# Kernel tuning notes

Hardware: AMD Instinct MI355X
Metric: run time of the kernel (lower is better)

Reference implementation:

```python
import jax, jax.numpy as jnp
import numpy as np

N = 100000
E = 800000
D = 128


def setup_inputs() -> dict:
    key = jax.random.key(0)
    k1, k2, k3, k4 = jax.random.split(key, 4)
    x = jax.random.normal(k1, (N, D), dtype=jnp.float32)
    edge_index = jax.random.randint(k2, (2, E), 0, N, dtype=jnp.int64)
    s = 1.0 / np.sqrt(D)
    W1 = jax.random.uniform(k3, (D, D), jnp.float32, -s, s)
    b1 = jnp.zeros((D,), jnp.float32)
    W2 = jax.random.uniform(k4, (D, D), jnp.float32, -s, s)
    b2 = jnp.zeros((D,), jnp.float32)
    return {"x": x, "edge_index": edge_index, "W1": W1, "b1": b1, "W2": W2, "b2": b2}


def _degree(idx, n, dtype):
    return jax.ops.segment_sum(jnp.ones(idx.shape, dtype), idx, num_segments=n)


def _graph_conv(x, row, col, W, b, residual, act):
    n = x.shape[0]
    deg_out = jnp.clip(_degree(row, n, x.dtype), 1.0)          # [N]
    x_src = x * jax.lax.rsqrt(deg_out)[:, None]                # [N, D]
    # scatter-add messages from source (row) into target (col)
    agg = jax.ops.segment_sum(x_src[row], col, num_segments=n)  # [N, D]
    out = agg @ W.T + b
    deg_in = jnp.clip(_degree(col, n, x.dtype), 1.0)
    out = out * jax.lax.rsqrt(deg_in)[:, None]
    if residual:
        out = out + x  # res_fc is Identity (in_dim == out_dim)
    if act:
        out = jax.nn.relu(out)
    return out


def reference(x, edge_index, W1, b1, W2, b2):
    row, col = edge_index[0], edge_index[1]
    # layer 1: relu + residual; layer 2 (last, encoding=False): no act, no residual
    h = _graph_conv(x, row, col, W1, b1, residual=True, act=True)
    h = _graph_conv(h, row, col, W2, b2, residual=False, act=False)
    return h
```

## Files before the change

### kernel.cpp

```cpp
#include <hip/hip_runtime.h>


#define NN 100000
#define EE 800000
#define DD 128
#define NB1 98
#define NTILE (NN / 16)

typedef __attribute__((ext_vector_type(8))) short short8;
typedef __attribute__((ext_vector_type(4))) float floatx4;

__device__ inline float bf2f(unsigned int u16) {
    union { unsigned int i; float f; } c;
    c.i = u16 << 16;
    return c.f;
}
__device__ inline ushort f2bf(float f) {
    union { float f; unsigned int i; } c;
    c.f = f;
    unsigned int u = c.i;
    return (ushort)((u + 0x7fffu + ((u >> 16) & 1u)) >> 16);
}

__global__ __launch_bounds__(256) void count_kernel(const int* __restrict__ row,
                                                    const int* __restrict__ col,
                                                    int* __restrict__ cnt_out,
                                                    int* __restrict__ cnt_in,
                                                    int* __restrict__ off) {
    int e = blockIdx.x * 256 + threadIdx.x;
    if (e < EE) {
        off[e] = atomicAdd(&cnt_in[col[e]], 1);
        atomicAdd(&cnt_out[row[e]], 1);
    }
}

__global__ __launch_bounds__(256) void dinv_kernel(const int* __restrict__ cnt_out,
                                                   const int* __restrict__ cnt_in,
                                                   float* __restrict__ dinv_out,
                                                   float* __restrict__ dinv_in) {
    int n = blockIdx.x * 256 + threadIdx.x;
    if (n < NN) {
        dinv_out[n] = rsqrtf((float)max(cnt_out[n], 1));
        dinv_in[n]  = rsqrtf((float)max(cnt_in[n], 1));
    }
}

__global__ __launch_bounds__(256) void scan1_kernel(const int* __restrict__ cnt,
                                                    int* __restrict__ excl,
                                                    int* __restrict__ bsums) {
    __shared__ int tmp[256];
    const int t = threadIdx.x;
    const int base = blockIdx.x * 1024 + t * 4;
    int a[4];
#pragma unroll
    for (int q = 0; q < 4; ++q) a[q] = (base + q < NN) ? cnt[base + q] : 0;
    int s = a[0] + a[1] + a[2] + a[3];
    tmp[t] = s;
    __syncthreads();
    for (int off = 1; off < 256; off <<= 1) {
        int v = 0;
        if (t >= off) v = tmp[t - off];
        __syncthreads();
        tmp[t] += v;
        __syncthreads();
    }
    int excl_s = tmp[t] - s;
    if (t == 255) bsums[blockIdx.x] = tmp[t];
    int run = excl_s;
#pragma unroll
    for (int q = 0; q < 4; ++q) {
        if (base + q < NN) excl[base + q] = run;
        run += a[q];
    }
}

__global__ __launch_bounds__(256) void scan2_kernel(int* __restrict__ bsums, int nb) {
    __shared__ int tmp[256];
    const int t = threadIdx.x;
    int s = (t < nb) ? bsums[t] : 0;
    tmp[t] = s;
    __syncthreads();
    for (int off = 1; off < 256; off <<= 1) {
        int v = 0;
        if (t >= off) v = tmp[t - off];
        __syncthreads();
        tmp[t] += v;
        __syncthreads();
    }
    if (t < nb) bsums[t] = tmp[t] - s;
}

__global__ __launch_bounds__(256) void scan3_kernel(const int* __restrict__ excl,
                                                    const int* __restrict__ bsums,
                                                    int* __restrict__ row_start) {
    int i = blockIdx.x * 256 + threadIdx.x;
    if (i < NN) row_start[i] = excl[i] + bsums[i >> 10];
}

__global__ __launch_bounds__(256) void fill_kernel(const int* __restrict__ row,
                                                   const int* __restrict__ col,
                                                   const int* __restrict__ row_start,
                                                   const int* __restrict__ off,
                                                   int* __restrict__ srcs) {
    int e = blockIdx.x * 256 + threadIdx.x;
    if (e < EE) srcs[row_start[col[e]] + off[e]] = row[e];
}

__global__ __launch_bounds__(256) void prescale_kernel(const float* __restrict__ x,
                                                       const float* __restrict__ dinv_out,
                                                       ushort* __restrict__ xb) {
    int idx = blockIdx.x * 256 + threadIdx.x;
    if (idx >= NN * 32) return;
    int n = idx >> 5;
    float s = dinv_out[n];
    float4 v = ((const float4*)x)[idx];
    ushort4 o;
    o.x = f2bf(v.x * s);
    o.y = f2bf(v.y * s);
    o.z = f2bf(v.z * s);
    o.w = f2bf(v.w * s);
    ((ushort4*)xb)[idx] = o;
}

__global__ __launch_bounds__(256) void gather_kernel(const ushort* __restrict__ src,
                                                     const int* __restrict__ row_start,
                                                     const int* __restrict__ srcs,
                                                     ushort* __restrict__ agg) {
    const int node = blockIdx.x * 16 + (threadIdx.x >> 4);
    const int lane = threadIdx.x & 15;
    if (node >= NN) return;
    int p = row_start[node];
    const int end = (node + 1 < NN) ? row_start[node + 1] : EE;
    float a0 = 0.f, a1 = 0.f, a2 = 0.f, a3 = 0.f;
    float a4 = 0.f, a5 = 0.f, a6 = 0.f, a7 = 0.f;

#define ACCUM(V)                                     \
    do {                                             \
        a0 += bf2f((V).x & 0xffffu);                 \
        a1 += bf2f((V).x >> 16);                     \
        a2 += bf2f((V).y & 0xffffu);                 \
        a3 += bf2f((V).y >> 16);                     \
        a4 += bf2f((V).z & 0xffffu);                 \
        a5 += bf2f((V).z >> 16);                     \
        a6 += bf2f((V).w & 0xffffu);                 \
        a7 += bf2f((V).w >> 16);                     \
    } while (0)

    for (; p + 3 < end; p += 4) {
        int s0 = srcs[p];
        int s1 = srcs[p + 1];
        int s2 = srcs[p + 2];
        int s3 = srcs[p + 3];
        uint4 v0 = ((const uint4*)(src + (size_t)s0 * DD))[lane];
        uint4 v1 = ((const uint4*)(src + (size_t)s1 * DD))[lane];
        uint4 v2 = ((const uint4*)(src + (size_t)s2 * DD))[lane];
        uint4 v3 = ((const uint4*)(src + (size_t)s3 * DD))[lane];
        ACCUM(v0); ACCUM(v1); ACCUM(v2); ACCUM(v3);
    }
    for (; p < end; ++p) {
        int s0 = srcs[p];
        uint4 v0 = ((const uint4*)(src + (size_t)s0 * DD))[lane];
        ACCUM(v0);
    }
#undef ACCUM

    uint4 o;
    o.x = (unsigned int)f2bf(a0) | ((unsigned int)f2bf(a1) << 16);
    o.y = (unsigned int)f2bf(a2) | ((unsigned int)f2bf(a3) << 16);
    o.z = (unsigned int)f2bf(a4) | ((unsigned int)f2bf(a5) << 16);
    o.w = (unsigned int)f2bf(a6) | ((unsigned int)f2bf(a7) << 16);
    ((uint4*)(agg + (size_t)node * DD))[lane] = o;
}

template <bool L1>
__global__ __launch_bounds__(256) void gemm_ep(const ushort* __restrict__ agg,
                                               const float* __restrict__ W,
                                               const float* __restrict__ bias,
                                               const float* __restrict__ dinv_in,
                                               const float* __restrict__ dinv_out,
                                               const float* __restrict__ x,
                                               ushort* __restrict__ hs,
                                               float* __restrict__ out) {
    __shared__ ushort Ws[128 * 136];
    {
        int j = threadIdx.x >> 1;
        int k0 = (threadIdx.x & 1) * 64;
        const float4* wp = (const float4*)(W + (size_t)j * DD + k0);
        ushort* dst = Ws + j * 136 + k0;
#pragma unroll
        for (int q = 0; q < 16; ++q) {
            float4 v = wp[q];
            ushort4 o;
            o.x = f2bf(v.x); o.y = f2bf(v.y); o.z = f2bf(v.z); o.w = f2bf(v.w);
            *(ushort4*)(dst + q * 4) = o;
        }
    }
    __syncthreads();

    const int wave = threadIdx.x >> 6;
    const int lane = threadIdx.x & 63;
    const int tile = blockIdx.x * 4 + wave;
    if (tile >= NTILE) return;
    const int mi = lane & 15;
    const int quad = lane >> 4;
    const int m0 = tile * 16;

    floatx4 acc[8];
#pragma unroll
    for (int t = 0; t < 8; ++t) acc[t] = (floatx4){0.f, 0.f, 0.f, 0.f};

    const ushort* ap = agg + (size_t)(m0 + mi) * DD + quad * 8;
#pragma unroll
    for (int s = 0; s < 4; ++s) {
        short8 a = *(const short8*)(ap + s * 32);
#pragma unroll
        for (int t = 0; t < 8; ++t) {
            short8 b = *(const short8*)(Ws + (t * 16 + mi) * 136 + s * 32 + quad * 8);
            acc[t] = __builtin_amdgcn_mfma_f32_16x16x32_bf16(a, b, acc[t], 0, 0, 0);
        }
    }

    float dv[4], dov[4];
#pragma unroll
    for (int i = 0; i < 4; ++i) {
        int r = m0 + quad * 4 + i;
        dv[i] = dinv_in[r];
        if (L1) dov[i] = dinv_out[r];
    }
#pragma unroll
    for (int t = 0; t < 8; ++t) {
        int c = t * 16 + mi;
        float bv = bias[c];
#pragma unroll
        for (int i = 0; i < 4; ++i) {
            int r = m0 + quad * 4 + i;
            float o = (acc[t][i] + bv) * dv[i];
            if (L1) {
                o += x[(size_t)r * DD + c];
                o = fmaxf(o, 0.f);
                hs[(size_t)r * DD + c] = f2bf(o * dov[i]);
            } else {
                out[(size_t)r * DD + c] = o;
            }
        }
    }
}

extern "C" void kernel_launch(void* const* d_in, const int* in_sizes, int n_in,
                              void* d_out, int out_size, void* d_ws, size_t ws_size,
                              hipStream_t stream) {
    const float* x  = (const float*)d_in[0];
    const int*   ei = (const int*)d_in[1];
    const float* W1 = (const float*)d_in[2];
    const float* b1 = (const float*)d_in[3];
    const float* W2 = (const float*)d_in[4];
    const float* b2 = (const float*)d_in[5];
    float* out = (float*)d_out;

    const int* row = ei;
    const int* col = ei + EE;

    ushort* agg     = (ushort*)d_ws;
    ushort* xb      = agg + (size_t)NN * DD;
    float* dinv_out = (float*)(xb + (size_t)NN * DD);
    float* dinv_in  = dinv_out + NN;
    int*   cnt      = (int*)(dinv_in + NN);
    int*   excl     = cnt + 2 * NN;
    int*   row_st   = excl + NN;
    int*   srcs     = row_st + NN;
    int*   bsums    = srcs + EE;
    int*   off      = (int*)agg;

    hipMemsetAsync(cnt, 0, 2 * NN * sizeof(int), stream);
    count_kernel<<<(EE + 255) / 256, 256, 0, stream>>>(row, col, cnt, cnt + NN, off);
    dinv_kernel<<<(NN + 255) / 256, 256, 0, stream>>>(cnt, cnt + NN, dinv_out, dinv_in);
    scan1_kernel<<<NB1, 256, 0, stream>>>(cnt + NN, excl, bsums);
    scan2_kernel<<<1, 256, 0, stream>>>(bsums, NB1);
    scan3_kernel<<<(NN + 255) / 256, 256, 0, stream>>>(excl, bsums, row_st);
    fill_kernel<<<(EE + 255) / 256, 256, 0, stream>>>(row, col, row_st, off, srcs);

    prescale_kernel<<<(NN * 32 + 255) / 256, 256, 0, stream>>>(x, dinv_out, xb);
    gather_kernel<<<(NN + 15) / 16, 256, 0, stream>>>(xb, row_st, srcs, agg);
    gemm_ep<true><<<(NTILE + 3) / 4, 256, 0, stream>>>(agg, W1, b1, dinv_in, dinv_out, x,
                                                       xb, nullptr);

    gather_kernel<<<(NN + 15) / 16, 256, 0, stream>>>(xb, row_st, srcs, agg);
    gemm_ep<false><<<(NTILE + 3) / 4, 256, 0, stream>>>(agg, W2, b2, dinv_in, nullptr, nullptr,
                                                        nullptr, out);
}
```

Baseline: 315.1 us.

## Fuse neighbor gather into GEMM epilogue kernel via shared-memory aggregation tile

Merges the gather kernel and the MFMA GEMM kernel into one per-layer kernel. Each block aggregates 64 destination rows into an LDS tile, then runs the bf16 MFMA GEMM from LDS. This removes the global round trip of the aggregation buffer and two launches, and layer 1 now writes into a separate hs buffer. The trade-off is higher LDS use per block, which lowers occupancy, and the whole block waits on its slowest gather row before the GEMM starts.

```diff
diff --git a/kernel.cpp b/kernel.cpp
--- a/kernel.cpp
+++ b/kernel.cpp
@@ -5,7 +5,6 @@
 #define EE 800000
 #define DD 128
 #define NB1 98
-#define NTILE (NN / 16)
 
 typedef __attribute__((ext_vector_type(8))) short short8;
 typedef __attribute__((ext_vector_type(4))) float floatx4;
@@ -122,66 +121,20 @@
     ((ushort4*)xb)[idx] = o;
 }
 
-__global__ __launch_bounds__(256) void gather_kernel(const ushort* __restrict__ src,
-                                                     const int* __restrict__ row_start,
-                                                     const int* __restrict__ srcs,
-                                                     ushort* __restrict__ agg) {
-    const int node = blockIdx.x * 16 + (threadIdx.x >> 4);
-    const int lane = threadIdx.x & 15;
-    if (node >= NN) return;
-    int p = row_start[node];
-    const int end = (node + 1 < NN) ? row_start[node + 1] : EE;
-    float a0 = 0.f, a1 = 0.f, a2 = 0.f, a3 = 0.f;
-    float a4 = 0.f, a5 = 0.f, a6 = 0.f, a7 = 0.f;
-
-#define ACCUM(V)                                     \
-    do {                                             \
-        a0 += bf2f((V).x & 0xffffu);                 \
-        a1 += bf2f((V).x >> 16);                     \
-        a2 += bf2f((V).y & 0xffffu);                 \
-        a3 += bf2f((V).y >> 16);                     \
-        a4 += bf2f((V).z & 0xffffu);                 \
-        a5 += bf2f((V).z >> 16);                     \
-        a6 += bf2f((V).w & 0xffffu);                 \
-        a7 += bf2f((V).w >> 16);                     \
-    } while (0)
-
-    for (; p + 3 < end; p += 4) {
-        int s0 = srcs[p];
-        int s1 = srcs[p + 1];
-        int s2 = srcs[p + 2];
-        int s3 = srcs[p + 3];
-        uint4 v0 = ((const uint4*)(src + (size_t)s0 * DD))[lane];
-        uint4 v1 = ((const uint4*)(src + (size_t)s1 * DD))[lane];
-        uint4 v2 = ((const uint4*)(src + (size_t)s2 * DD))[lane];
-        uint4 v3 = ((const uint4*)(src + (size_t)s3 * DD))[lane];
-        ACCUM(v0); ACCUM(v1); ACCUM(v2); ACCUM(v3);
-    }
-    for (; p < end; ++p) {
-        int s0 = srcs[p];
-        uint4 v0 = ((const uint4*)(src + (size_t)s0 * DD))[lane];
-        ACCUM(v0);
-    }
-#undef ACCUM
-
-    uint4 o;
-    o.x = (unsigned int)f2bf(a0) | ((unsigned int)f2bf(a1) << 16);
-    o.y = (unsigned int)f2bf(a2) | ((unsigned int)f2bf(a3) << 16);
-    o.z = (unsigned int)f2bf(a4) | ((unsigned int)f2bf(a5) << 16);
-    o.w = (unsigned int)f2bf(a6) | ((unsigned int)f2bf(a7) << 16);
-    ((uint4*)(agg + (size_t)node * DD))[lane] = o;
-}
-
 template <bool L1>
-__global__ __launch_bounds__(256) void gemm_ep(const ushort* __restrict__ agg,
-                                               const float* __restrict__ W,
-                                               const float* __restrict__ bias,
-                                               const float* __restrict__ dinv_in,
-                                               const float* __restrict__ dinv_out,
-                                               const float* __restrict__ x,
-                                               ushort* __restrict__ hs,
-                                               float* __restrict__ out) {
+__global__ __launch_bounds__(256) void fused_layer(const ushort* __restrict__ src,
+                                                   const int* __restrict__ row_start,
+                                                   const int* __restrict__ srcs,
+                                                   const float* __restrict__ W,
+                                                   const float* __restrict__ bias,
+                                                   const float* __restrict__ dinv_in,
+                                                   const float* __restrict__ dinv_out,
+                                                   const float* __restrict__ x,
+                                                   ushort* __restrict__ hs,
+                                                   float* __restrict__ out) {
     __shared__ ushort Ws[128 * 136];
+    __shared__ ushort At[64 * 136];
+
     {
         int j = threadIdx.x >> 1;
         int k0 = (threadIdx.x & 1) * 64;
@@ -195,21 +148,68 @@
             *(ushort4*)(dst + q * 4) = o;
         }
     }
+
+    {
+        const int grp  = threadIdx.x >> 4;
+        const int lane = threadIdx.x & 15;
+        const int m0 = blockIdx.x * 64;
+        for (int q = 0; q < 4; ++q) {
+            const int node = m0 + q * 16 + grp;
+            float a0 = 0.f, a1 = 0.f, a2 = 0.f, a3 = 0.f;
+            float a4 = 0.f, a5 = 0.f, a6 = 0.f, a7 = 0.f;
+            if (node < NN) {
+                int p = row_start[node];
+                const int end = (node + 1 < NN) ? row_start[node + 1] : EE;
+#define ACCUM(V)                                 \
+    do {                                         \
+        a0 += bf2f((V).x & 0xffffu);             \
+        a1 += bf2f((V).x >> 16);                 \
+        a2 += bf2f((V).y & 0xffffu);             \
+        a3 += bf2f((V).y >> 16);                 \
+        a4 += bf2f((V).z & 0xffffu);             \
+        a5 += bf2f((V).z >> 16);                 \
+        a6 += bf2f((V).w & 0xffffu);             \
+        a7 += bf2f((V).w >> 16);                 \
+    } while (0)
+                for (; p + 3 < end; p += 4) {
+                    int s0 = srcs[p];
+                    int s1 = srcs[p + 1];
+                    int s2 = srcs[p + 2];
+                    int s3 = srcs[p + 3];
+                    uint4 v0 = ((const uint4*)(src + (size_t)s0 * DD))[lane];
+                    uint4 v1 = ((const uint4*)(src + (size_t)s1 * DD))[lane];
+                    uint4 v2 = ((const uint4*)(src + (size_t)s2 * DD))[lane];
+                    uint4 v3 = ((const uint4*)(src + (size_t)s3 * DD))[lane];
+                    ACCUM(v0); ACCUM(v1); ACCUM(v2); ACCUM(v3);
+                }
+                for (; p < end; ++p) {
+                    int s0 = srcs[p];
+                    uint4 v0 = ((const uint4*)(src + (size_t)s0 * DD))[lane];
+                    ACCUM(v0);
+                }
+#undef ACCUM
+            }
+            uint4 o;
+            o.x = (unsigned int)f2bf(a0) | ((unsigned int)f2bf(a1) << 16);
+            o.y = (unsigned int)f2bf(a2) | ((unsigned int)f2bf(a3) << 16);
+            o.z = (unsigned int)f2bf(a4) | ((unsigned int)f2bf(a5) << 16);
+            o.w = (unsigned int)f2bf(a6) | ((unsigned int)f2bf(a7) << 16);
+            *(uint4*)(At + (q * 16 + grp) * 136 + lane * 8) = o;
+        }
+    }
     __syncthreads();
 
     const int wave = threadIdx.x >> 6;
     const int lane = threadIdx.x & 63;
-    const int tile = blockIdx.x * 4 + wave;
-    if (tile >= NTILE) return;
     const int mi = lane & 15;
     const int quad = lane >> 4;
-    const int m0 = tile * 16;
+    const int m0 = blockIdx.x * 64 + wave * 16;
 
     floatx4 acc[8];
 #pragma unroll
     for (int t = 0; t < 8; ++t) acc[t] = (floatx4){0.f, 0.f, 0.f, 0.f};
 
-    const ushort* ap = agg + (size_t)(m0 + mi) * DD + quad * 8;
+    const ushort* ap = At + (wave * 16 + mi) * 136 + quad * 8;
 #pragma unroll
     for (int s = 0; s < 4; ++s) {
         short8 a = *(const short8*)(ap + s * 32);
@@ -224,8 +224,9 @@
 #pragma unroll
     for (int i = 0; i < 4; ++i) {
         int r = m0 + quad * 4 + i;
-        dv[i] = dinv_in[r];
-        if (L1) dov[i] = dinv_out[r];
+        int rc = r < NN ? r : (NN - 1);
+        dv[i] = dinv_in[rc];
+        if (L1) dov[i] = dinv_out[rc];
     }
 #pragma unroll
     for (int t = 0; t < 8; ++t) {
@@ -234,13 +235,15 @@
 #pragma unroll
         for (int i = 0; i < 4; ++i) {
             int r = m0 + quad * 4 + i;
-            float o = (acc[t][i] + bv) * dv[i];
-            if (L1) {
-                o += x[(size_t)r * DD + c];
-                o = fmaxf(o, 0.f);
-                hs[(size_t)r * DD + c] = f2bf(o * dov[i]);
-            } else {
-                out[(size_t)r * DD + c] = o;
+            if (r < NN) {
+                float o = (acc[t][i] + bv) * dv[i];
+                if (L1) {
+                    o += x[(size_t)r * DD + c];
+                    o = fmaxf(o, 0.f);
+                    hs[(size_t)r * DD + c] = f2bf(o * dov[i]);
+                } else {
+                    out[(size_t)r * DD + c] = o;
+                }
             }
         }
     }
@@ -260,16 +263,16 @@
     const int* row = ei;
     const int* col = ei + EE;
 
-    ushort* agg     = (ushort*)d_ws;
-    ushort* xb      = agg + (size_t)NN * DD;
-    float* dinv_out = (float*)(xb + (size_t)NN * DD);
+    ushort* xb      = (ushort*)d_ws;
+    ushort* hs      = xb + (size_t)NN * DD;
+    int*    off     = (int*)hs;
+    float* dinv_out = (float*)(hs + (size_t)NN * DD);
     float* dinv_in  = dinv_out + NN;
     int*   cnt      = (int*)(dinv_in + NN);
     int*   excl     = cnt + 2 * NN;
     int*   row_st   = excl + NN;
     int*   srcs     = row_st + NN;
     int*   bsums    = srcs + EE;
-    int*   off      = (int*)agg;
 
     hipMemsetAsync(cnt, 0, 2 * NN * sizeof(int), stream);
     count_kernel<<<(EE + 255) / 256, 256, 0, stream>>>(row, col, cnt, cnt + NN, off);
@@ -280,11 +283,9 @@
     fill_kernel<<<(EE + 255) / 256, 256, 0, stream>>>(row, col, row_st, off, srcs);
 
     prescale_kernel<<<(NN * 32 + 255) / 256, 256, 0, stream>>>(x, dinv_out, xb);
-    gather_kernel<<<(NN + 15) / 16, 256, 0, stream>>>(xb, row_st, srcs, agg);
-    gemm_ep<true><<<(NTILE + 3) / 4, 256, 0, stream>>>(agg, W1, b1, dinv_in, dinv_out, x,
-                                                       xb, nullptr);
-
-    gather_kernel<<<(NN + 15) / 16, 256, 0, stream>>>(xb, row_st, srcs, agg);
-    gemm_ep<false><<<(NTILE + 3) / 4, 256, 0, stream>>>(agg, W2, b2, dinv_in, nullptr, nullptr,
-                                                        nullptr, out);
-}
+    fused_layer<true><<<(NN + 63) / 64, 256, 0, stream>>>(xb, row_st, srcs, W1, b1,
+                                                          dinv_in, dinv_out, x, hs, nullptr);
+
+    fused_layer<false><<<(NN + 63) / 64, 256, 0, stream>>>(hs, row_st, srcs, W2, b2,
+                                                           dinv_in, nullptr, nullptr, nullptr, out);
+}
```

After: 370.9 us. 1.18x slower.

## Fuse degree counting with bf16 cast and merge scan stages with dinv computation

Applied to the files above, without the earlier changes.

The per-source out-degree scaling moves out of the prescale pass and into the gather, so the x-to-bf16 cast no longer depends on degrees and can run in the same launch as edge counting. Scan phases 2 and 3 and the dinv computation are merged into one kernel that redundantly scans the block sums in every block. row_start gains a sentinel entry so the gather bounds check is simpler. The aim is fewer kernel launches and less serialization, at the cost of an extra dinv_out load per edge and extra multiplies in the gather.

```diff
diff --git a/kernel.cpp b/kernel.cpp
--- a/kernel.cpp
+++ b/kernel.cpp
@@ -5,6 +5,8 @@
 #define EE 800000
 #define DD 128
 #define NB1 98
+#define CB  3125
+#define XB  12500
 #define NTILE (NN / 16)
 
 typedef __attribute__((ext_vector_type(8))) short short8;
@@ -22,26 +24,24 @@
     return (ushort)((u + 0x7fffu + ((u >> 16) & 1u)) >> 16);
 }
 
-__global__ __launch_bounds__(256) void count_kernel(const int* __restrict__ row,
-                                                    const int* __restrict__ col,
-                                                    int* __restrict__ cnt_out,
-                                                    int* __restrict__ cnt_in,
-                                                    int* __restrict__ off) {
-    int e = blockIdx.x * 256 + threadIdx.x;
-    if (e < EE) {
+__global__ __launch_bounds__(256) void countcast_kernel(const int* __restrict__ row,
+                                                        const int* __restrict__ col,
+                                                        int* __restrict__ cnt_out,
+                                                        int* __restrict__ cnt_in,
+                                                        int* __restrict__ off,
+                                                        const float* __restrict__ x,
+                                                        ushort* __restrict__ xb) {
+    const int b = blockIdx.x;
+    if (b < CB) {
+        int e = b * 256 + threadIdx.x;
         off[e] = atomicAdd(&cnt_in[col[e]], 1);
         atomicAdd(&cnt_out[row[e]], 1);
-    }
-}
-
-__global__ __launch_bounds__(256) void dinv_kernel(const int* __restrict__ cnt_out,
-                                                   const int* __restrict__ cnt_in,
-                                                   float* __restrict__ dinv_out,
-                                                   float* __restrict__ dinv_in) {
-    int n = blockIdx.x * 256 + threadIdx.x;
-    if (n < NN) {
-        dinv_out[n] = rsqrtf((float)max(cnt_out[n], 1));
-        dinv_in[n]  = rsqrtf((float)max(cnt_in[n], 1));
+    } else {
+        int idx = (b - CB) * 256 + threadIdx.x;
+        float4 v = ((const float4*)x)[idx];
+        ushort4 o;
+        o.x = f2bf(v.x); o.y = f2bf(v.y); o.z = f2bf(v.z); o.w = f2bf(v.w);
+        ((ushort4*)xb)[idx] = o;
     }
 }
 
@@ -74,27 +74,36 @@
     }
 }
 
-__global__ __launch_bounds__(256) void scan2_kernel(int* __restrict__ bsums, int nb) {
-    __shared__ int tmp[256];
+__global__ __launch_bounds__(256) void scanB_kernel(const int* __restrict__ excl,
+                                                    const int* __restrict__ bsums,
+                                                    const int* __restrict__ cnt_out,
+                                                    const int* __restrict__ cnt_in,
+                                                    int* __restrict__ row_start,
+                                                    float* __restrict__ dinv_out,
+                                                    float* __restrict__ dinv_in) {
+    __shared__ int tmp[128];
     const int t = threadIdx.x;
-    int s = (t < nb) ? bsums[t] : 0;
-    tmp[t] = s;
+    if (t < 128) tmp[t] = (t < NB1) ? bsums[t] : 0;
     __syncthreads();
-    for (int off = 1; off < 256; off <<= 1) {
+    for (int off = 1; off < 128; off <<= 1) {
         int v = 0;
-        if (t >= off) v = tmp[t - off];
-        __syncthreads();
-        tmp[t] += v;
-        __syncthreads();
-    }
-    if (t < nb) bsums[t] = tmp[t] - s;
-}
-
-__global__ __launch_bounds__(256) void scan3_kernel(const int* __restrict__ excl,
-                                                    const int* __restrict__ bsums,
-                                                    int* __restrict__ row_start) {
-    int i = blockIdx.x * 256 + threadIdx.x;
-    if (i < NN) row_start[i] = excl[i] + bsums[i >> 10];
+        if (t < 128 && t >= off) v = tmp[t - off];
+        __syncthreads();
+        if (t < 128) tmp[t] += v;
+        __syncthreads();
+    }
+    const int base = (blockIdx.x == 0) ? 0 : tmp[blockIdx.x - 1];
+    const int i0 = blockIdx.x * 1024 + t * 4;
+#pragma unroll
+    for (int q = 0; q < 4; ++q) {
+        int i = i0 + q;
+        if (i < NN) {
+            row_start[i] = excl[i] + base;
+            dinv_in[i]  = rsqrtf((float)max(cnt_in[i], 1));
+            dinv_out[i] = rsqrtf((float)max(cnt_out[i], 1));
+        }
+    }
+    if (blockIdx.x == 0 && t == 0) row_start[NN] = EE;
 }
 
 __global__ __launch_bounds__(256) void fill_kernel(const int* __restrict__ row,
@@ -106,44 +115,29 @@
     if (e < EE) srcs[row_start[col[e]] + off[e]] = row[e];
 }
 
-__global__ __launch_bounds__(256) void prescale_kernel(const float* __restrict__ x,
-                                                       const float* __restrict__ dinv_out,
-                                                       ushort* __restrict__ xb) {
-    int idx = blockIdx.x * 256 + threadIdx.x;
-    if (idx >= NN * 32) return;
-    int n = idx >> 5;
-    float s = dinv_out[n];
-    float4 v = ((const float4*)x)[idx];
-    ushort4 o;
-    o.x = f2bf(v.x * s);
-    o.y = f2bf(v.y * s);
-    o.z = f2bf(v.z * s);
-    o.w = f2bf(v.w * s);
-    ((ushort4*)xb)[idx] = o;
-}
-
 __global__ __launch_bounds__(256) void gather_kernel(const ushort* __restrict__ src,
                                                      const int* __restrict__ row_start,
                                                      const int* __restrict__ srcs,
+                                                     const float* __restrict__ dinv_out,
                                                      ushort* __restrict__ agg) {
     const int node = blockIdx.x * 16 + (threadIdx.x >> 4);
     const int lane = threadIdx.x & 15;
     if (node >= NN) return;
     int p = row_start[node];
-    const int end = (node + 1 < NN) ? row_start[node + 1] : EE;
+    const int end = row_start[node + 1];
     float a0 = 0.f, a1 = 0.f, a2 = 0.f, a3 = 0.f;
     float a4 = 0.f, a5 = 0.f, a6 = 0.f, a7 = 0.f;
 
-#define ACCUM(V)                                     \
+#define ACCUM(V, C)                                  \
     do {                                             \
-        a0 += bf2f((V).x & 0xffffu);                 \
-        a1 += bf2f((V).x >> 16);                     \
-        a2 += bf2f((V).y & 0xffffu);                 \
-        a3 += bf2f((V).y >> 16);                     \
-        a4 += bf2f((V).z & 0xffffu);                 \
-        a5 += bf2f((V).z >> 16);                     \
-        a6 += bf2f((V).w & 0xffffu);                 \
-        a7 += bf2f((V).w >> 16);                     \
+        a0 += bf2f((V).x & 0xffffu) * (C);           \
+        a1 += bf2f((V).x >> 16) * (C);               \
+        a2 += bf2f((V).y & 0xffffu) * (C);           \
+        a3 += bf2f((V).y >> 16) * (C);               \
+        a4 += bf2f((V).z & 0xffffu) * (C);           \
+        a5 += bf2f((V).z >> 16) * (C);               \
+        a6 += bf2f((V).w & 0xffffu) * (C);           \
+        a7 += bf2f((V).w >> 16) * (C);               \
     } while (0)
 
     for (; p + 3 < end; p += 4) {
@@ -151,16 +145,21 @@
         int s1 = srcs[p + 1];
         int s2 = srcs[p + 2];
         int s3 = srcs[p + 3];
+        float c0 = dinv_out[s0];
+        float c1 = dinv_out[s1];
+        float c2 = dinv_out[s2];
+        float c3 = dinv_out[s3];
         uint4 v0 = ((const uint4*)(src + (size_t)s0 * DD))[lane];
         uint4 v1 = ((const uint4*)(src + (size_t)s1 * DD))[lane];
         uint4 v2 = ((const uint4*)(src + (size_t)s2 * DD))[lane];
         uint4 v3 = ((const uint4*)(src + (size_t)s3 * DD))[lane];
-        ACCUM(v0); ACCUM(v1); ACCUM(v2); ACCUM(v3);
+        ACCUM(v0, c0); ACCUM(v1, c1); ACCUM(v2, c2); ACCUM(v3, c3);
     }
     for (; p < end; ++p) {
         int s0 = srcs[p];
+        float c0 = dinv_out[s0];
         uint4 v0 = ((const uint4*)(src + (size_t)s0 * DD))[lane];
-        ACCUM(v0);
+        ACCUM(v0, c0);
     }
 #undef ACCUM
 
@@ -177,9 +176,8 @@
                                                const float* __restrict__ W,
                                                const float* __restrict__ bias,
                                                const float* __restrict__ dinv_in,
-                                               const float* __restrict__ dinv_out,
                                                const float* __restrict__ x,
-                                               ushort* __restrict__ hs,
+                                               ushort* __restrict__ hb,
                                                float* __restrict__ out) {
     __shared__ ushort Ws[128 * 136];
     {
@@ -220,13 +218,9 @@
         }
     }
 
-    float dv[4], dov[4];
-#pragma unroll
-    for (int i = 0; i < 4; ++i) {
-        int r = m0 + quad * 4 + i;
-        dv[i] = dinv_in[r];
-        if (L1) dov[i] = dinv_out[r];
-    }
+    float dv[4];
+#pragma unroll
+    for (int i = 0; i < 4; ++i) dv[i] = dinv_in[m0 + quad * 4 + i];
 #pragma unroll
     for (int t = 0; t < 8; ++t) {
         int c = t * 16 + mi;
@@ -238,7 +232,7 @@
             if (L1) {
                 o += x[(size_t)r * DD + c];
                 o = fmaxf(o, 0.f);
-                hs[(size_t)r * DD + c] = f2bf(o * dov[i]);
+                hb[(size_t)r * DD + c] = f2bf(o);
             } else {
                 out[(size_t)r * DD + c] = o;
             }
@@ -262,29 +256,26 @@
 
     ushort* agg     = (ushort*)d_ws;
     ushort* xb      = agg + (size_t)NN * DD;
+    ushort* hb      = xb;
+    int*    off     = (int*)agg;
     float* dinv_out = (float*)(xb + (size_t)NN * DD);
     float* dinv_in  = dinv_out + NN;
     int*   cnt      = (int*)(dinv_in + NN);
     int*   excl     = cnt + 2 * NN;
     int*   row_st   = excl + NN;
-    int*   srcs     = row_st + NN;
+    int*   srcs     = row_st + NN + 1;
     int*   bsums    = srcs + EE;
-    int*   off      = (int*)agg;
 
     hipMemsetAsync(cnt, 0, 2 * NN * sizeof(int), stream);
-    count_kernel<<<(EE + 255) / 256, 256, 0, stream>>>(row, col, cnt, cnt + NN, off);
-    dinv_kernel<<<(NN + 255) / 256, 256, 0, stream>>>(cnt, cnt + NN, dinv_out, dinv_in);
+    countcast_kernel<<<CB + XB, 256, 0, stream>>>(row, col, cnt, cnt + NN, off, x, xb);
     scan1_kernel<<<NB1, 256, 0, stream>>>(cnt + NN, excl, bsums);
-    scan2_kernel<<<1, 256, 0, stream>>>(bsums, NB1);
-    scan3_kernel<<<(NN + 255) / 256, 256, 0, stream>>>(excl, bsums, row_st);
+    scanB_kernel<<<NB1, 256, 0, stream>>>(excl, bsums, cnt, cnt + NN, row_st,
+                                          dinv_out, dinv_in);
     fill_kernel<<<(EE + 255) / 256, 256, 0, stream>>>(row, col, row_st, off, srcs);
 
-    prescale_kernel<<<(NN * 32 + 255) / 256, 256, 0, stream>>>(x, dinv_out, xb);
-    gather_kernel<<<(NN + 15) / 16, 256, 0, stream>>>(xb, row_st, srcs, agg);
-    gemm_ep<true><<<(NTILE + 3) / 4, 256, 0, stream>>>(agg, W1, b1, dinv_in, dinv_out, x,
-                                                       xb, nullptr);
-
-    gather_kernel<<<(NN + 15) / 16, 256, 0, stream>>>(xb, row_st, srcs, agg);
-    gemm_ep<false><<<(NTILE + 3) / 4, 256, 0, stream>>>(agg, W2, b2, dinv_in, nullptr, nullptr,
-                                                        nullptr, out);
-}
+    gather_kernel<<<(NN + 15) / 16, 256, 0, stream>>>(xb, row_st, srcs, dinv_out, agg);
+    gemm_ep<true><<<(NTILE + 3) / 4, 256, 0, stream>>>(agg, W1, b1, dinv_in, x, hb, nullptr);
+
+    gather_kernel<<<(NN + 15) / 16, 256, 0, stream>>>(hb, row_st, srcs, dinv_out, agg);
+    gemm_ep<false><<<(NTILE + 3) / 4, 256, 0, stream>>>(agg, W2, b2, dinv_in, nullptr, nullptr, out);
+}
```

Result: no change. 316.7 us (+0.5%).
